# Kernel tuning notes

Hardware: AMD Instinct MI355X
Metric: run time of the kernel (lower is better)

## Reference

```python
import jax, jax.numpy as jnp
import numpy as np
from jax import lax

G = 8  # number of RBF grid points (FastKAN default style)
GRID = jnp.linspace(-2.0, 2.0, G)
DENOM = 4.0 / (G - 1)  # grid spacing used as gaussian width


def _fastkan_conv(x, ln_w, ln_b, Wb, bb, Ws):
    # x: [B, C, H, W]; 3x3 conv, stride 1, pad 1 via patch unfold + FastKAN linear
    B, C, H, W = x.shape
    p = lax.conv_general_dilated_patches(x, (3, 3), (1, 1), ((1, 1), (1, 1)))  # [B, C*9, H, W]
    p = p.transpose(0, 2, 3, 1).reshape(B * H * W, C * 9)  # [N, in]
    # LayerNorm over patch features (FastKAN normalizes before the RBF basis)
    mu = p.mean(-1, keepdims=True)
    var = p.var(-1, keepdims=True)
    pn = (p - mu) / jnp.sqrt(var + 1e-5) * ln_w + ln_b
    # Gaussian RBF basis: [N, in, G]
    rbf = jnp.exp(-jnp.square((pn[:, :, None] - GRID) / DENOM))
    spline = rbf.reshape(B * H * W, -1) @ Ws.T          # [N, out]
    base = jax.nn.silu(p) @ Wb.T + bb                    # [N, out]
    out = spline + base
    return out.reshape(B, H, W, -1).transpose(0, 3, 1, 2)  # [B, out, H, W]


def _bn_relu_pool(h, gamma, beta):
    # BatchNorm2d in training mode (batch stats), ReLU, MaxPool2d(2,2)
    mu = h.mean((0, 2, 3), keepdims=True)
    var = h.var((0, 2, 3), keepdims=True)
    h = (h - mu) / jnp.sqrt(var + 1e-5) * gamma[None, :, None, None] + beta[None, :, None, None]
    h = jax.nn.relu(h)
    return lax.reduce_window(h, -jnp.inf, lax.max, (1, 1, 2, 2), (1, 1, 2, 2), 'VALID')


def setup_inputs() -> dict:
    key = jax.random.key(0)
    ks = jax.random.split(key, 16)
    B, Cin, H, W = 32, 16, 64, 64
    dims = [(Cin * 9, 64), (64 * 9, 128), (128 * 9, 256)]
    inp = {"x": jax.random.normal(ks[0], (B, Cin, H, W), jnp.float32)}
    for i, (fin, fout) in enumerate(dims, 1):
        inp[f"ln_w{i}"] = jnp.ones((fin,), jnp.float32)
        inp[f"ln_b{i}"] = jnp.zeros((fin,), jnp.float32)
        inp[f"Wb{i}"] = jax.random.normal(ks[3 * i], (fout, fin), jnp.float32) * 0.05
        inp[f"bb{i}"] = jnp.zeros((fout,), jnp.float32)
        inp[f"Ws{i}"] = jax.random.normal(ks[3 * i + 1], (fout, fin * G), jnp.float32) * 0.05
        inp[f"g{i}"] = jnp.ones((fout,), jnp.float32)
        inp[f"be{i}"] = jnp.zeros((fout,), jnp.float32)
    return inp


def reference(x, ln_w1, ln_b1, Wb1, bb1, Ws1, g1, be1,
              ln_w2, ln_b2, Wb2, bb2, Ws2, g2, be2,
              ln_w3, ln_b3, Wb3, bb3, Ws3, g3, be3):
    h = _bn_relu_pool(_fastkan_conv(x, ln_w1, ln_b1, Wb1, bb1, Ws1), g1, be1)
    h = _bn_relu_pool(_fastkan_conv(h, ln_w2, ln_b2, Wb2, bb2, Ws2), g2, be2)
    h = _bn_relu_pool(_fastkan_conv(h, ln_w3, ln_b3, Wb3, bb3, Ws3), g3, be3)
    return h.reshape(h.shape[0], -1)  # flatten: [B, 256*8*8]
```

## Files before the change

### kernel.cpp

```cpp
#include <hip/hip_runtime.h>

typedef _Float16 half_t;
typedef __attribute__((ext_vector_type(8))) _Float16 half8;
typedef __attribute__((ext_vector_type(4))) float floatx4;


#define RBF_SCALE 2.1019644f
#define RBF_G0   -4.2039288f
#define RBF_2D    2.40224482f
#define RBF_D2    1.44269504f
#define RBF_Q     0.13533528f
#define LOG2E     1.44269504f

template<int C, int H, int W>
__global__ __launch_bounds__(256)
void ln_prep(const float* __restrict__ x,
             const float* __restrict__ lnw, const float* __restrict__ lnb,
             half_t* __restrict__ pn, half_t* __restrict__ sp)
{
    const int HW = H * W, IN = C * 9, CH = IN / 8;
    const int NL = (IN + 63) / 64;
    __shared__ float xw[C * 57];
    __shared__ short offs[C * 9];
    __shared__ float2 pms[16];

    const int wv = threadIdx.x >> 6, lane = threadIdx.x & 63;
    const int pix0 = blockIdx.x * 16;
    const int b = pix0 / HW, hw0 = pix0 % HW;
    const int h = hw0 / W, x0 = hw0 % W;
    const float* xb = x + (long)b * C * HW;

    for (int idx = threadIdx.x; idx < C * 54; idx += 256) {
        int ch = idx / 54, rem = idx - ch * 54;
        int dy = rem / 18, col = rem - dy * 18;
        int y = h + dy - 1, xx = x0 + col - 1;
        float v = 0.f;
        if (y >= 0 && y < H && xx >= 0 && xx < W)
            v = xb[(long)ch * HW + y * W + xx];
        xw[ch * 57 + dy * 19 + col] = v;
    }
    for (int i = threadIdx.x; i < IN; i += 256) {
        int ch = i / 9, r = i - ch * 9;
        int dy = r / 3, dx = r - dy * 3;
        offs[i] = (short)(ch * 57 + dy * 19 + dx);
    }
    __syncthreads();

    #pragma unroll
    for (int p = 0; p < 4; ++p) {
        const int px = wv * 4 + p;
        float s = 0.f, s2 = 0.f;
        #pragma unroll
        for (int t = 0; t < NL; ++t) {
            int i = t * 64 + lane;
            if (i < IN) {
                float v = xw[offs[i] + px];
                s += v; s2 += v * v;
            }
        }
        #pragma unroll
        for (int off = 32; off > 0; off >>= 1) {
            s  += __shfl_down(s,  off, 64);
            s2 += __shfl_down(s2, off, 64);
        }
        if (lane == 0) {
            float mean = s / IN;
            float istd = rsqrtf(s2 / IN - mean * mean + 1e-5f);
            pms[px] = make_float2(mean, istd);
        }
    }
    __syncthreads();

    const int TOT = 16 * CH;
    for (int c = threadIdx.x; c < TOT; c += 256) {
        int p = c / CH, q = c - p * CH;
        float2 msv = pms[p];
        const float mean = msv.x, istd = msv.y;
        const int i0 = q * 8;
        float4 w0 = *(const float4*)(lnw + i0);
        float4 w1 = *(const float4*)(lnw + i0 + 4);
        float4 b0 = *(const float4*)(lnb + i0);
        float4 b1 = *(const float4*)(lnb + i0 + 4);
        float lw[8] = {w0.x, w0.y, w0.z, w0.w, w1.x, w1.y, w1.z, w1.w};
        float lb[8] = {b0.x, b0.y, b0.z, b0.w, b1.x, b1.y, b1.z, b1.w};
        half8 a, s8;
        #pragma unroll
        for (int e = 0; e < 8; ++e) {
            float val = xw[offs[i0 + e] + p];
            float pnv = fmaf((val - mean) * istd, lw[e], lb[e]) * RBF_SCALE;
            pnv = fminf(12.f, fmaxf(-12.f, pnv));
            a[e] = (half_t)pnv;
            float ev = __builtin_amdgcn_exp2f(-val * LOG2E);
            s8[e] = (half_t)(val * __builtin_amdgcn_rcpf(1.f + ev));
        }
        const long base = (long)(pix0 + p) * IN + i0;
        *(half8*)&pn[base] = a;
        *(half8*)&sp[base] = s8;
    }
}

template<int IN, int OUT>
__global__ __launch_bounds__(256)
void conv_w(const float* __restrict__ Ws, const float* __restrict__ Wb,
            half_t* __restrict__ Wt)
{
    const int NIB = (IN + 63) / 64, NSTEP = NIB * 9;
    int idx = blockIdx.x * 256 + threadIdx.x;
    if (idx >= OUT * NSTEP * 64) return;
    int uu = idx & 63;
    int t = idx >> 6;
    int o = t % OUT;
    int s = t / OUT;
    int iblk = s / 9, j = s % 9;
    int ulin = (((uu >> 3) ^ (o & 7)) << 3) + (uu & 7);
    int i = iblk * 64 + ulin;
    float v = 0.f;
    if (i < IN)
        v = (j < 8) ? Ws[(long)o * IN * 8 + i * 8 + j] : Wb[(long)o * IN + i];
    Wt[idx] = (half_t)v;
}

template<int IN, int OUT, int HW, int NB, int SPLIT>
__global__ __launch_bounds__(256)
void kan_gemm(const half_t* __restrict__ pn, const half_t* __restrict__ sp,
              const half_t* __restrict__ Wt, float* __restrict__ out)
{
    const int NIB = (IN + 63) / 64;

    __shared__ half_t As[64 * 64];
    __shared__ half_t Bs[NB * 64 * 64];

    const int tid = threadIdx.x;
    const int row = tid >> 2, q = tid & 3;
    const int pix = blockIdx.x * 64 + row;
    const half_t* pnrow = pn + (long)pix * IN;
    const half_t* sprow = sp + (long)pix * IN;

    const int wv = tid >> 6, lane = tid & 63;
    const int lr = lane & 15, lq = lane >> 4;
    const int u0 = (2 * q) ^ (row & 7);
    const int u1 = (2 * q + 1) ^ (row & 7);
    const int yoff = blockIdx.y * (4 * NB * 16);

    floatx4 acc[NB][4] = {};
    float r[16], u[16];
    half8 pf0, pf1;

    const int grpA = (blockIdx.z * NIB) / SPLIT;
    const int grpB = ((blockIdx.z + 1) * NIB) / SPLIT;
    const int s0 = grpA * 9, s1 = grpB * 9;

    int jg = 0, ibg = grpA;

    auto ldglob = [&](const half_t* base, int ib, half8& a, half8& b) {
        int i0 = ib * 64 + q * 16;
        const half_t* pp = base + ((i0 < IN) ? i0 : 0);
        a = *(const half8*)pp;
        b = *(const half8*)(pp + 8);
    };

    auto stageB = [&](int it) {
        const half_t* wsrc = Wt + (long)it * OUT * 64
                              + (long)(yoff + wv * NB * 16) * 64;
        #pragma unroll
        for (int c = 0; c < NB * 2; ++c) {
            __builtin_amdgcn_global_load_lds(
                (const __attribute__((address_space(1))) void*)(wsrc + c * 512 + lane * 8),
                (__attribute__((address_space(3))) void*)(&Bs[wv * NB * 1024 + c * 512]),
                16, 0, 0);
        }
    };

    auto genA = [&]() {
        if (jg < 8) {
            if (jg == 0) {
                #pragma unroll
                for (int kk = 0; kk < 8; ++kk) {
                    float d0 = (float)pf0[kk] - RBF_G0;
                    float d1 = (float)pf1[kk] - RBF_G0;
                    r[kk]     = __builtin_amdgcn_exp2f(-(d0 * d0));
                    u[kk]     = __builtin_amdgcn_exp2f(fmaf(RBF_2D, d0, -RBF_D2));
                    r[kk + 8] = __builtin_amdgcn_exp2f(-(d1 * d1));
                    u[kk + 8] = __builtin_amdgcn_exp2f(fmaf(RBF_2D, d1, -RBF_D2));
                }
            }
            half8 a0, a1;
            #pragma unroll
            for (int kk = 0; kk < 8; ++kk) {
                a0[kk] = (half_t)r[kk];
                a1[kk] = (half_t)r[kk + 8];
            }
            *(half8*)&As[row * 64 + u0 * 8] = a0;
            *(half8*)&As[row * 64 + u1 * 8] = a1;
            if (jg < 7) {
                #pragma unroll
                for (int kk = 0; kk < 16; ++kk) { r[kk] *= u[kk]; u[kk] *= RBF_Q; }
            }
            if (jg == 7) ldglob(sprow, ibg, pf0, pf1);
        } else {
            *(half8*)&As[row * 64 + u0 * 8] = pf0;
            *(half8*)&As[row * 64 + u1 * 8] = pf1;
            ldglob(pnrow, ibg + 1, pf0, pf1);
        }
        if (++jg == 9) { jg = 0; ++ibg; }
    };

    auto domfma = [&]() {
        __builtin_amdgcn_s_setprio(1);
        #pragma unroll
        for (int ks = 0; ks < 2; ++ks) {
            half8 af[4], bf[NB];
            #pragma unroll
            for (int mf = 0; mf < 4; ++mf) {
                int rr = mf * 16 + lr;
                af[mf] = *(const half8*)&As[rr * 64 + (((ks * 4 + lq) ^ (rr & 7)) * 8)];
            }
            #pragma unroll
            for (int nb = 0; nb < NB; ++nb) {
                int rr = wv * NB * 16 + nb * 16 + lr;
                bf[nb] = *(const half8*)&Bs[rr * 64 + (((ks * 4 + lq) ^ (rr & 7)) * 8)];
            }
            #pragma unroll
            for (int nb = 0; nb < NB; ++nb)
                #pragma unroll
                for (int mf = 0; mf < 4; ++mf)
                    acc[nb][mf] = __builtin_amdgcn_mfma_f32_16x16x32_f16(
                        bf[nb], af[mf], acc[nb][mf], 0, 0, 0);
        }
        __builtin_amdgcn_s_setprio(0);
    };

    ldglob(pnrow, grpA, pf0, pf1);

    for (int it = s0; it < s1; ++it) {
        __syncthreads();
        stageB(it);
        genA();
        __syncthreads();
        domfma();
    }

    const long zoff = (long)blockIdx.z * ((long)gridDim.x * 64) * OUT;
    #pragma unroll
    for (int nb = 0; nb < NB; ++nb)
    #pragma unroll
    for (int mf = 0; mf < 4; ++mf)
    #pragma unroll
    for (int reg = 0; reg < 4; ++reg) {
        int o  = yoff + wv * NB * 16 + nb * 16 + lq * 4 + reg;
        int p2 = blockIdx.x * 64 + mf * 16 + lr;
        int b2 = p2 / HW, hw2 = p2 % HW;
        out[zoff + ((long)b2 * OUT + o) * HW + hw2] = acc[nb][mf][reg];
    }
}

__launch_bounds__(256)
__global__ void bn_stats(const float* __restrict__ h, const float* __restrict__ bias,
                         int C, int HW, int B, int nz, float* __restrict__ sums)
{
    int c = blockIdx.y;
    float bbc = bias[c];
    long zstride = (long)B * C * HW;
    int hw4 = HW / 4;
    int total4 = B * hw4;
    float s = 0.f, s2 = 0.f;
    for (int idx = blockIdx.x * 256 + threadIdx.x; idx < total4; idx += 256 * gridDim.x) {
        int b = idx / hw4, r4 = idx - b * hw4;
        long base = ((long)b * C + c) * HW + (long)r4 * 4;
        float4 a = make_float4(bbc, bbc, bbc, bbc);
        for (int z = 0; z < nz; ++z) {
            float4 p = *(const float4*)&h[z * zstride + base];
            a.x += p.x; a.y += p.y; a.z += p.z; a.w += p.w;
        }
        s  += a.x + a.y + a.z + a.w;
        s2 += a.x * a.x + a.y * a.y + a.z * a.z + a.w * a.w;
    }
    for (int off = 32; off > 0; off >>= 1) {
        s  += __shfl_down(s,  off, 64);
        s2 += __shfl_down(s2, off, 64);
    }
    __shared__ float rs[4], rs2[4];
    int lane = threadIdx.x & 63, wid = threadIdx.x >> 6;
    if (lane == 0) { rs[wid] = s; rs2[wid] = s2; }
    __syncthreads();
    if (threadIdx.x == 0) {
        atomicAdd(&sums[c],     rs[0] + rs[1] + rs[2] + rs[3]);
        atomicAdd(&sums[C + c], rs2[0] + rs2[1] + rs2[2] + rs2[3]);
    }
}

__launch_bounds__(256)
__global__ void bn_relu_pool(const float* __restrict__ h, const float* __restrict__ sums,
                             const float* __restrict__ bias,
                             const float* __restrict__ gamma, const float* __restrict__ beta,
                             float* __restrict__ out, int B, int C, int H, int W, int nz)
{
    int Ho = H / 2, Wo = W / 2, Wo4 = Wo / 4;
    long total4 = (long)B * C * Ho * Wo4;
    long idx = (long)blockIdx.x * 256 + threadIdx.x;
    if (idx >= total4) return;
    int pw4 = idx % Wo4; long t = idx / Wo4;
    int ph = t % Ho; t /= Ho;
    int c = t % C; int b = (int)(t / C);
    int pw0 = pw4 * 4;

    float M = (float)B * H * W;
    float mean = sums[c] / M;
    float var  = sums[C + c] / M - mean * mean;
    float scale = gamma[c] * rsqrtf(var + 1e-5f);
    float shift = beta[c] - mean * scale + bias[c] * scale;

    long zstride = (long)B * C * H * W;
    const float* hp = h + ((long)b * C + c) * H * W;
    long off0 = (long)(2 * ph) * W + 2 * pw0;
    long off1 = off0 + W;

    float4 r0a = make_float4(0.f, 0.f, 0.f, 0.f), r0b = r0a, r1a = r0a, r1b = r0a;
    for (int z = 0; z < nz; ++z) {
        const float* hz = hp + z * zstride;
        float4 p;
        p = *(const float4*)&hz[off0];     r0a.x += p.x; r0a.y += p.y; r0a.z += p.z; r0a.w += p.w;
        p = *(const float4*)&hz[off0 + 4]; r0b.x += p.x; r0b.y += p.y; r0b.z += p.z; r0b.w += p.w;
        p = *(const float4*)&hz[off1];     r1a.x += p.x; r1a.y += p.y; r1a.z += p.z; r1a.w += p.w;
        p = *(const float4*)&hz[off1 + 4]; r1b.x += p.x; r1b.y += p.y; r1b.z += p.z; r1b.w += p.w;
    }

    float e[8];
    e[0]=fmaf(r0a.x,scale,shift); e[1]=fmaf(r0a.y,scale,shift);
    e[2]=fmaf(r0a.z,scale,shift); e[3]=fmaf(r0a.w,scale,shift);
    e[4]=fmaf(r0b.x,scale,shift); e[5]=fmaf(r0b.y,scale,shift);
    e[6]=fmaf(r0b.z,scale,shift); e[7]=fmaf(r0b.w,scale,shift);
    float f[8];
    f[0]=fmaf(r1a.x,scale,shift); f[1]=fmaf(r1a.y,scale,shift);
    f[2]=fmaf(r1a.z,scale,shift); f[3]=fmaf(r1a.w,scale,shift);
    f[4]=fmaf(r1b.x,scale,shift); f[5]=fmaf(r1b.y,scale,shift);
    f[6]=fmaf(r1b.z,scale,shift); f[7]=fmaf(r1b.w,scale,shift);

    float4 o4;
    o4.x = fmaxf(0.f, fmaxf(fmaxf(e[0], e[1]), fmaxf(f[0], f[1])));
    o4.y = fmaxf(0.f, fmaxf(fmaxf(e[2], e[3]), fmaxf(f[2], f[3])));
    o4.z = fmaxf(0.f, fmaxf(fmaxf(e[4], e[5]), fmaxf(f[4], f[5])));
    o4.w = fmaxf(0.f, fmaxf(fmaxf(e[6], e[7]), fmaxf(f[6], f[7])));

    long obase = (((long)b * C + c) * Ho + ph) * Wo + pw0;
    *(float4*)&out[obase] = o4;
}

extern "C" void kernel_launch(void* const* d_in, const int* in_sizes, int n_in,
                              void* d_out, int out_size, void* d_ws, size_t ws_size,
                              hipStream_t stream) {
    const float* x     = (const float*)d_in[0];
    const float* ln_w1 = (const float*)d_in[1];  const float* ln_b1 = (const float*)d_in[2];
    const float* Wb1   = (const float*)d_in[3];  const float* bb1   = (const float*)d_in[4];
    const float* Ws1   = (const float*)d_in[5];  const float* g1    = (const float*)d_in[6];
    const float* be1   = (const float*)d_in[7];
    const float* ln_w2 = (const float*)d_in[8];  const float* ln_b2 = (const float*)d_in[9];
    const float* Wb2   = (const float*)d_in[10]; const float* bb2   = (const float*)d_in[11];
    const float* Ws2   = (const float*)d_in[12]; const float* g2    = (const float*)d_in[13];
    const float* be2   = (const float*)d_in[14];
    const float* ln_w3 = (const float*)d_in[15]; const float* ln_b3 = (const float*)d_in[16];
    const float* Wb3   = (const float*)d_in[17]; const float* bb3   = (const float*)d_in[18];
    const float* Ws3   = (const float*)d_in[19]; const float* g3    = (const float*)d_in[20];
    const float* be3   = (const float*)d_in[21];

    const int B = 32;
    char* ws = (char*)d_ws;
    float*  convbuf = (float*)(ws + 0);
    float*  poolbuf = (float*)(ws + 33554432);
    float*  stats1  = (float*)(ws + 41943040);
    float*  stats2  = (float*)(ws + 41945088);
    float*  stats3  = (float*)(ws + 41947136);
    half_t* wt1     = (half_t*)(ws + 41949184);
    half_t* wt2     = (half_t*)(ws + 42170368);
    half_t* wt3     = (half_t*)(ws + 43497472);
    half_t* pnbuf   = (half_t*)(ws + 48805888);
    half_t* spbuf   = (half_t*)(ws + 86554624);

    hipMemsetAsync(stats1, 0, 6144, stream);

    conv_w<144, 64><<<(64 * 27 * 64 + 255) / 256, 256, 0, stream>>>(Ws1, Wb1, wt1);
    conv_w<576, 128><<<(128 * 81 * 64 + 255) / 256, 256, 0, stream>>>(Ws2, Wb2, wt2);
    conv_w<1152, 256><<<(256 * 162 * 64 + 255) / 256, 256, 0, stream>>>(Ws3, Wb3, wt3);

    {
        const int H = 64, W = 64, OUT = 64;
        int npix = B * H * W;
        ln_prep<16, H, W><<<npix / 16, 256, 0, stream>>>(x, ln_w1, ln_b1, pnbuf, spbuf);
        kan_gemm<144, OUT, H * W, 1, 1><<<dim3(npix / 64, 1, 1), 256, 0, stream>>>(
            pnbuf, spbuf, wt1, convbuf);
        bn_stats<<<dim3(64, OUT), 256, 0, stream>>>(convbuf, bb1, OUT, H * W, B, 1, stats1);
        long tot4 = (long)B * OUT * (H / 2) * (W / 2) / 4;
        bn_relu_pool<<<(tot4 + 255) / 256, 256, 0, stream>>>(
            convbuf, stats1, bb1, g1, be1, poolbuf, B, OUT, H, W, 1);
    }
    {
        const int H = 32, W = 32, OUT = 128;
        int npix = B * H * W;
        ln_prep<64, H, W><<<npix / 16, 256, 0, stream>>>(poolbuf, ln_w2, ln_b2, pnbuf, spbuf);
        kan_gemm<576, OUT, H * W, 2, 2><<<dim3(npix / 64, 1, 2), 256, 0, stream>>>(
            pnbuf, spbuf, wt2, convbuf);
        bn_stats<<<dim3(16, OUT), 256, 0, stream>>>(convbuf, bb2, OUT, H * W, B, 2, stats2);
        long tot4 = (long)B * OUT * (H / 2) * (W / 2) / 4;
        bn_relu_pool<<<(tot4 + 255) / 256, 256, 0, stream>>>(
            convbuf, stats2, bb2, g2, be2, poolbuf, B, OUT, H, W, 2);
    }
    {
        const int H = 16, W = 16, OUT = 256;
        int npix = B * H * W;
        ln_prep<128, H, W><<<npix / 16, 256, 0, stream>>>(poolbuf, ln_w3, ln_b3, pnbuf, spbuf);
        kan_gemm<1152, OUT, H * W, 2, 4><<<dim3(npix / 64, 2, 4), 256, 0, stream>>>(
            pnbuf, spbuf, wt3, convbuf);
        bn_stats<<<dim3(8, OUT), 256, 0, stream>>>(convbuf, bb3, OUT, H * W, B, 4, stats3);
        long tot4 = (long)B * OUT * (H / 2) * (W / 2) / 4;
        bn_relu_pool<<<(tot4 + 255) / 256, 256, 0, stream>>>(
            convbuf, stats3, bb3, g3, be3, (float*)d_out, B, OUT, H, W, 4);
    }
}
```

Baseline: 453.2 us.

## Fuse BN-ReLU-pool into next layer's LN prep and merge weight packing

The separate bn_relu_pool launches for layers 1 and 2 are removed. The next layer's patch-prep kernel now reads the raw conv output, sums the split-K partials, and applies BN scale/shift, ReLU and 2x2 max-pool while filling its shared-memory window. The memset and three weight-packing kernels are also merged into one prep_all launch. This cuts launches and skips the write and reread of the pooled intermediate. In exchange, each conv element is re-read by overlapping 3x3 windows and the prep kernel does more work per block.

```diff
diff --git a/kernel.cpp b/kernel.cpp
--- a/kernel.cpp
+++ b/kernel.cpp
@@ -99,25 +99,152 @@
     }
 }
 
-template<int IN, int OUT>
+template<int C, int H, int W, int NZ>
 __global__ __launch_bounds__(256)
-void conv_w(const float* __restrict__ Ws, const float* __restrict__ Wb,
-            half_t* __restrict__ Wt)
-{
-    const int NIB = (IN + 63) / 64, NSTEP = NIB * 9;
-    int idx = blockIdx.x * 256 + threadIdx.x;
-    if (idx >= OUT * NSTEP * 64) return;
-    int uu = idx & 63;
-    int t = idx >> 6;
-    int o = t % OUT;
-    int s = t / OUT;
+void ln_prep_bn(const float* __restrict__ conv, const float* __restrict__ sums,
+                const float* __restrict__ bias, const float* __restrict__ gamma,
+                const float* __restrict__ beta,
+                const float* __restrict__ lnw, const float* __restrict__ lnb,
+                half_t* __restrict__ pn, half_t* __restrict__ sp)
+{
+    const int HW = H * W, IN = C * 9, CH = IN / 8;
+    const int NL = (IN + 63) / 64;
+    const int Hc = 2 * H, Wc = 2 * W;
+    __shared__ float xw[C * 57];
+    __shared__ short offs[C * 9];
+    __shared__ float2 pms[16];
+    __shared__ float scl[C], shf[C];
+
+    const int wv = threadIdx.x >> 6, lane = threadIdx.x & 63;
+    const int pix0 = blockIdx.x * 16;
+    const int b = pix0 / HW, hw0 = pix0 % HW;
+    const int h = hw0 / W, x0 = hw0 % W;
+
+    for (int c = threadIdx.x; c < C; c += 256) {
+        float M = 32.f * Hc * Wc;
+        float mean = sums[c] / M;
+        float var  = sums[C + c] / M - mean * mean;
+        float scale = gamma[c] * rsqrtf(var + 1e-5f);
+        scl[c] = scale;
+        shf[c] = beta[c] - mean * scale + bias[c] * scale;
+    }
+    __syncthreads();
+
+    const long zstride = 32L * C * Hc * Wc;
+    const float* cb = conv + (long)b * C * Hc * Wc;
+
+    for (int idx = threadIdx.x; idx < C * 54; idx += 256) {
+        int ch = idx / 54, rem = idx - ch * 54;
+        int dy = rem / 18, col = rem - dy * 18;
+        int py = h + dy - 1, px = x0 + col - 1;
+        float v = 0.f;
+        if (py >= 0 && py < H && px >= 0 && px < W) {
+            long base = (long)ch * Hc * Wc + (long)(2 * py) * Wc + 2 * px;
+            float s00 = 0.f, s01 = 0.f, s10 = 0.f, s11 = 0.f;
+            #pragma unroll
+            for (int z = 0; z < NZ; ++z) {
+                const float* p = cb + z * zstride + base;
+                float2 r0 = *(const float2*)&p[0];
+                float2 r1 = *(const float2*)&p[Wc];
+                s00 += r0.x; s01 += r0.y; s10 += r1.x; s11 += r1.y;
+            }
+            float sc = scl[ch], sh = shf[ch];
+            v = fmaxf(0.f, fmaxf(fmaxf(fmaf(s00, sc, sh), fmaf(s01, sc, sh)),
+                                 fmaxf(fmaf(s10, sc, sh), fmaf(s11, sc, sh))));
+        }
+        xw[ch * 57 + dy * 19 + col] = v;
+    }
+    for (int i = threadIdx.x; i < IN; i += 256) {
+        int ch = i / 9, r = i - ch * 9;
+        int dy = r / 3, dx = r - dy * 3;
+        offs[i] = (short)(ch * 57 + dy * 19 + dx);
+    }
+    __syncthreads();
+
+    #pragma unroll
+    for (int p = 0; p < 4; ++p) {
+        const int px = wv * 4 + p;
+        float s = 0.f, s2 = 0.f;
+        #pragma unroll
+        for (int t = 0; t < NL; ++t) {
+            int i = t * 64 + lane;
+            if (i < IN) {
+                float v = xw[offs[i] + px];
+                s += v; s2 += v * v;
+            }
+        }
+        #pragma unroll
+        for (int off = 32; off > 0; off >>= 1) {
+            s  += __shfl_down(s,  off, 64);
+            s2 += __shfl_down(s2, off, 64);
+        }
+        if (lane == 0) {
+            float mean = s / IN;
+            float istd = rsqrtf(s2 / IN - mean * mean + 1e-5f);
+            pms[px] = make_float2(mean, istd);
+        }
+    }
+    __syncthreads();
+
+    const int TOT = 16 * CH;
+    for (int c = threadIdx.x; c < TOT; c += 256) {
+        int p = c / CH, q = c - p * CH;
+        float2 msv = pms[p];
+        const float mean = msv.x, istd = msv.y;
+        const int i0 = q * 8;
+        float4 w0 = *(const float4*)(lnw + i0);
+        float4 w1 = *(const float4*)(lnw + i0 + 4);
+        float4 b0 = *(const float4*)(lnb + i0);
+        float4 b1 = *(const float4*)(lnb + i0 + 4);
+        float lw[8] = {w0.x, w0.y, w0.z, w0.w, w1.x, w1.y, w1.z, w1.w};
+        float lb[8] = {b0.x, b0.y, b0.z, b0.w, b1.x, b1.y, b1.z, b1.w};
+        half8 a, s8;
+        #pragma unroll
+        for (int e = 0; e < 8; ++e) {
+            float val = xw[offs[i0 + e] + p];
+            float pnv = fmaf((val - mean) * istd, lw[e], lb[e]) * RBF_SCALE;
+            pnv = fminf(12.f, fmaxf(-12.f, pnv));
+            a[e] = (half_t)pnv;
+            float ev = __builtin_amdgcn_exp2f(-val * LOG2E);
+            s8[e] = (half_t)(val * __builtin_amdgcn_rcpf(1.f + ev));
+        }
+        const long base = (long)(pix0 + p) * IN + i0;
+        *(half8*)&pn[base] = a;
+        *(half8*)&sp[base] = s8;
+    }
+}
+
+__device__ __forceinline__ void pack_one(long t, int IN, int OUT,
+                                         const float* __restrict__ Ws,
+                                         const float* __restrict__ Wb,
+                                         half_t* __restrict__ Wt)
+{
+    int uu = (int)(t & 63);
+    long r = t >> 6;
+    int o = (int)(r % OUT);
+    int s = (int)(r / OUT);
     int iblk = s / 9, j = s % 9;
     int ulin = (((uu >> 3) ^ (o & 7)) << 3) + (uu & 7);
     int i = iblk * 64 + ulin;
     float v = 0.f;
     if (i < IN)
         v = (j < 8) ? Ws[(long)o * IN * 8 + i * 8 + j] : Wb[(long)o * IN + i];
-    Wt[idx] = (half_t)v;
+    Wt[t] = (half_t)v;
+}
+
+__launch_bounds__(256)
+__global__ void prep_all(const float* __restrict__ Ws1, const float* __restrict__ Wb1,
+                         const float* __restrict__ Ws2, const float* __restrict__ Wb2,
+                         const float* __restrict__ Ws3, const float* __restrict__ Wb3,
+                         half_t* __restrict__ wt1, half_t* __restrict__ wt2,
+                         half_t* __restrict__ wt3, float* __restrict__ stats)
+{
+    const long n1 = 64L * 27 * 64, n2 = 128L * 81 * 64, n3 = 256L * 162 * 64;
+    long idx = (long)blockIdx.x * 256 + threadIdx.x;
+    if (idx < 1536) stats[idx] = 0.f;
+    if (idx < n1)                 pack_one(idx,            144,  64, Ws1, Wb1, wt1);
+    else if (idx < n1 + n2)       pack_one(idx - n1,       576, 128, Ws2, Wb2, wt2);
+    else if (idx < n1 + n2 + n3)  pack_one(idx - n1 - n2, 1152, 256, Ws3, Wb3, wt3);
 }
 
 template<int IN, int OUT, int HW, int NB, int SPLIT>
@@ -366,7 +493,6 @@
     const int B = 32;
     char* ws = (char*)d_ws;
     float*  convbuf = (float*)(ws + 0);
-    float*  poolbuf = (float*)(ws + 33554432);
     float*  stats1  = (float*)(ws + 41943040);
     float*  stats2  = (float*)(ws + 41945088);
     float*  stats3  = (float*)(ws + 41947136);
@@ -376,11 +502,11 @@
     half_t* pnbuf   = (half_t*)(ws + 48805888);
     half_t* spbuf   = (half_t*)(ws + 86554624);
 
-    hipMemsetAsync(stats1, 0, 6144, stream);
-
-    conv_w<144, 64><<<(64 * 27 * 64 + 255) / 256, 256, 0, stream>>>(Ws1, Wb1, wt1);
-    conv_w<576, 128><<<(128 * 81 * 64 + 255) / 256, 256, 0, stream>>>(Ws2, Wb2, wt2);
-    conv_w<1152, 256><<<(256 * 162 * 64 + 255) / 256, 256, 0, stream>>>(Ws3, Wb3, wt3);
+    {
+        const long n = 64L*27*64 + 128L*81*64 + 256L*162*64;
+        prep_all<<<(int)((n + 255) / 256), 256, 0, stream>>>(
+            Ws1, Wb1, Ws2, Wb2, Ws3, Wb3, wt1, wt2, wt3, stats1);
+    }
 
     {
         const int H = 64, W = 64, OUT = 64;
@@ -389,30 +515,26 @@
         kan_gemm<144, OUT, H * W, 1, 1><<<dim3(npix / 64, 1, 1), 256, 0, stream>>>(
             pnbuf, spbuf, wt1, convbuf);
         bn_stats<<<dim3(64, OUT), 256, 0, stream>>>(convbuf, bb1, OUT, H * W, B, 1, stats1);
-        long tot4 = (long)B * OUT * (H / 2) * (W / 2) / 4;
-        bn_relu_pool<<<(tot4 + 255) / 256, 256, 0, stream>>>(
-            convbuf, stats1, bb1, g1, be1, poolbuf, B, OUT, H, W, 1);
     }
     {
         const int H = 32, W = 32, OUT = 128;
         int npix = B * H * W;
-        ln_prep<64, H, W><<<npix / 16, 256, 0, stream>>>(poolbuf, ln_w2, ln_b2, pnbuf, spbuf);
+        ln_prep_bn<64, H, W, 1><<<npix / 16, 256, 0, stream>>>(
+            convbuf, stats1, bb1, g1, be1, ln_w2, ln_b2, pnbuf, spbuf);
         kan_gemm<576, OUT, H * W, 2, 2><<<dim3(npix / 64, 1, 2), 256, 0, stream>>>(
             pnbuf, spbuf, wt2, convbuf);
         bn_stats<<<dim3(16, OUT), 256, 0, stream>>>(convbuf, bb2, OUT, H * W, B, 2, stats2);
-        long tot4 = (long)B * OUT * (H / 2) * (W / 2) / 4;
-        bn_relu_pool<<<(tot4 + 255) / 256, 256, 0, stream>>>(
-            convbuf, stats2, bb2, g2, be2, poolbuf, B, OUT, H, W, 2);
     }
     {
         const int H = 16, W = 16, OUT = 256;
         int npix = B * H * W;
-        ln_prep<128, H, W><<<npix / 16, 256, 0, stream>>>(poolbuf, ln_w3, ln_b3, pnbuf, spbuf);
+        ln_prep_bn<128, H, W, 2><<<npix / 16, 256, 0, stream>>>(
+            convbuf, stats2, bb2, g2, be2, ln_w3, ln_b3, pnbuf, spbuf);
         kan_gemm<1152, OUT, H * W, 2, 4><<<dim3(npix / 64, 2, 4), 256, 0, stream>>>(
             pnbuf, spbuf, wt3, convbuf);
         bn_stats<<<dim3(8, OUT), 256, 0, stream>>>(convbuf, bb3, OUT, H * W, B, 4, stats3);
-        long tot4 = (long)B * OUT * (H / 2) * (W / 2) / 4;
-        bn_relu_pool<<<(tot4 + 255) / 256, 256, 0, stream>>>(
+        bn_relu_pool<<<(int)(((long)B * OUT * (H / 2) * (W / 2) / 4 + 255) / 256),
+                       256, 0, stream>>>(
             convbuf, stats3, bb3, g3, be3, (float*)d_out, B, OUT, H, W, 4);
     }
 }
```

Measured after the change: 451.5 us. No clear change (-0.4%).
